# Performance work log

Measured on AMD Instinct MI355X. Metric: run time of the kernel, lower is better.

The kernel has to match this reference:

```python
import jax, jax.numpy as jnp
import numpy as np

B, T, S, D, H = 4, 1024, 1024, 1024, 16
DH = D // H  # head dim = 64
EPS = 1e-5
NEG = -1e9  # finite stand-in for -inf (grad-safe)


def setup_inputs() -> dict:
    key = jax.random.key(0)
    ks = jax.random.split(key, 9)
    std = D ** -0.5
    return {
        "q": jax.random.normal(ks[0], (B, T, D), jnp.float32),
        "k": jax.random.normal(ks[1], (B, S, D), jnp.float32),
        "v": jax.random.normal(ks[2], (B, S, D), jnp.float32),
        "attn_mask": jax.random.randint(ks[3], (T, S), 0, 2) == 1,
        "attn_bias": jax.random.normal(ks[4], (H, T, S), jnp.float32) * 0.1,
        "Wq": jax.random.normal(ks[5], (D, D), jnp.float32) * std,
        "Wk": jax.random.normal(ks[6], (D, D), jnp.float32) * std,
        "Wv": jax.random.normal(ks[7], (D, D), jnp.float32) * std,
        "Wo": jax.random.normal(ks[8], (D, D), jnp.float32) * std,
    }


def reference(q, k, v, attn_mask, attn_bias, Wq, Wk, Wv, Wo):
    # project and split heads: [B,T,D] -> [B,H,T,DH]
    qh = (q @ Wq.T).reshape(B, T, H, DH).transpose(0, 2, 1, 3) * (DH ** -0.5)
    kh = (k @ Wk.T).reshape(B, S, H, DH).transpose(0, 2, 1, 3)
    vh = (v @ Wv.T).reshape(B, S, H, DH).transpose(0, 2, 1, 3)
    # scores [B,H,T,S] with bias broadcast over batch, mask over (B,H)
    attn = jnp.einsum('bhtd,bhsd->bhts', qh, kh) + attn_bias
    attn = jnp.where(attn_mask, NEG, attn)
    # inverted softmax: normalize jointly over (heads, target) for each source pos
    a = jax.nn.softmax(attn.reshape(B, H * T, S), axis=1).reshape(B, H, T, S)
    a = jnp.where(attn_mask, 0.0, a)
    a = a / (a.sum(axis=-1, keepdims=True) + EPS)
    out = jnp.einsum('bhts,bhsd->bhtd', a, vh).transpose(0, 2, 1, 3).reshape(B, T, D)
    return out @ Wo.T
```

## Files before the change

### kernel.cpp

```cpp
#include <hip/hip_runtime.h>
#include <hip/hip_bf16.h>
#include <math.h>
#include <stdint.h>

#define B_ 4
#define T_ 1024
#define S_ 1024
#define D_ 1024
#define H_ 16
#define DH_ 64

static constexpr float EPSV = 1e-5f;
static constexpr float LOG2E = 1.4426950408889634f;
static constexpr float NEG2 = -1.4426950e9f;
static constexpr float SCALE_Q = 0.125f * LOG2E;

typedef __attribute__((ext_vector_type(8))) short short8;
typedef __attribute__((ext_vector_type(4))) float f32x4;

#define MFMA_BF16 __builtin_amdgcn_mfma_f32_16x16x32_bf16

__device__ __forceinline__ ushort f2bf(float f) {
  union { float f; unsigned u; } v; v.f = f;
  unsigned r = (v.u + 0x7FFFu + ((v.u >> 16) & 1u)) >> 16;
  return (ushort)r;
}
__device__ __forceinline__ float bf2f(ushort u) {
  union { unsigned u; float f; } v; v.u = (unsigned)u << 16;
  return v.f;
}
__device__ __forceinline__ float exp2_fast(float x) {
  float r;
  asm("v_exp_f32 %0, %1" : "=v"(r) : "v"(x));
  return r;
}
__device__ __forceinline__ unsigned cvt_pk_bf16(float lo, float hi) {
  unsigned r;
  asm("v_cvt_pk_bf16_f32 %0, %1, %2" : "=v"(r) : "v"(lo), "v"(hi));
  return r;
}

__device__ __forceinline__ void gl_lds16(const ushort* g, ushort* l) {
  __builtin_amdgcn_global_load_lds(
      (const __attribute__((address_space(1))) unsigned int*)g,
      (__attribute__((address_space(3))) unsigned int*)l, 16, 0, 0);
}

__global__ __launch_bounds__(256) void k_prep(
    const float* __restrict__ q, const float* __restrict__ k,
    const float* __restrict__ v, const float* __restrict__ Wq,
    const float* __restrict__ Wk, const float* __restrict__ Wv,
    const float* __restrict__ Wo, const float* __restrict__ bias,
    const int* __restrict__ mask, ushort* __restrict__ qb,
    ushort* __restrict__ kb, ushort* __restrict__ vb,
    ushort* __restrict__ Wqb, ushort* __restrict__ Wkb,
    ushort* __restrict__ Wvb, ushort* __restrict__ Wob,
    ushort* __restrict__ bm) {
  const int tid = threadIdx.x;
#pragma unroll 4
  for (int it = 0; it < 16; ++it) {
    const int tile = blockIdx.x + (it << 11);
    if (tile < 16384) {
      const float* src;
      ushort* dst;
      int local;
      if (tile < 12288) {
        const int which = tile >> 12;
        local = tile & 4095;
        src = (which == 0) ? q : (which == 1) ? k : v;
        dst = (which == 0) ? qb : (which == 1) ? kb : vb;
      } else {
        const int wv_ = tile - 12288;
        const int which = wv_ >> 10;
        local = wv_ & 1023;
        src = (which == 0) ? Wq : (which == 1) ? Wk : (which == 2) ? Wv : Wo;
        dst = (which == 0) ? Wqb : (which == 1) ? Wkb : (which == 2) ? Wvb : Wob;
      }
      const size_t base = (size_t)local * 1024 + tid * 4;
      float4 f = *(const float4*)(src + base);
      *(ushort4*)(dst + base) =
          make_ushort4(f2bf(f.x), f2bf(f.y), f2bf(f.z), f2bf(f.w));
    } else {
      const size_t base = (size_t)(tile - 16384) * 1024 + tid * 4;
      const size_t mi = base & (size_t)(T_ * S_ - 1);
      float4 b0 = *(const float4*)(bias + base);
      int4 m0 = *(const int4*)(mask + mi);
      ushort4 o = make_ushort4(f2bf(m0.x ? NEG2 : b0.x * LOG2E),
                               f2bf(m0.y ? NEG2 : b0.y * LOG2E),
                               f2bf(m0.z ? NEG2 : b0.z * LOG2E),
                               f2bf(m0.w ? NEG2 : b0.w * LOG2E));
      *(ushort4*)(bm + base) = o;
    }
  }
}

template <int MODE>
__global__ __launch_bounds__(256) void k_gemm(const ushort* __restrict__ A,
                                              const ushort* __restrict__ W,
                                              void* __restrict__ Yv,
                                              float scale) {
  __shared__ ushort At[128][32];
  __shared__ ushort Wt[128][32];
  const int tid = threadIdx.x;
  const int l = tid & 63, w = tid >> 6;
  const int wm = (w >> 1) * 64, wn = (w & 1) * 64;
  const int r16 = l & 15, g = l >> 4;
  const int i0 = blockIdx.x * 128, j0 = blockIdx.y * 128;
  const int srow = (l >> 2), scol = (l & 3) << 3;
  f32x4 acc[4][4] = {};

  for (int k0 = 0; k0 < D_; k0 += 32) {
    __syncthreads();
#pragma unroll
    for (int u = 0; u < 2; ++u) {
      const int row = w * 32 + u * 16 + srow;
      gl_lds16(&A[(size_t)(i0 + row) * D_ + k0 + scol], &At[w * 32 + u * 16][0]);
      gl_lds16(&W[(size_t)(j0 + row) * D_ + k0 + scol], &Wt[w * 32 + u * 16][0]);
    }
    __syncthreads();
    short8 a0[4], b0[4];
#pragma unroll
    for (int i = 0; i < 4; ++i) a0[i] = *(const short8*)&At[wm + 16 * i + r16][g * 8];
#pragma unroll
    for (int j = 0; j < 4; ++j) b0[j] = *(const short8*)&Wt[wn + 16 * j + r16][g * 8];
#pragma unroll
    for (int i = 0; i < 4; ++i)
#pragma unroll
      for (int j = 0; j < 4; ++j)
        acc[i][j] = MFMA_BF16(a0[i], b0[j], acc[i][j], 0, 0, 0);
  }

#pragma unroll
  for (int i = 0; i < 4; ++i)
#pragma unroll
    for (int j = 0; j < 4; ++j) {
      if (MODE == 2) {
        const int row0 = i0 + wm + 16 * i + 4 * g;
        const int col = j0 + wn + 16 * j + r16;
        const int bb = row0 >> 10, s = row0 & 1023;
        const int hh = col >> 6, dh = col & 63;
        ushort4 pw;
        pw.x = f2bf(acc[i][j][0] * scale); pw.y = f2bf(acc[i][j][1] * scale);
        pw.z = f2bf(acc[i][j][2] * scale); pw.w = f2bf(acc[i][j][3] * scale);
        *(ushort4*)&((ushort*)Yv)[((size_t)(bb * H_ + hh) * DH_ + dh) * 1024 + s] = pw;
      } else {
#pragma unroll
        for (int r = 0; r < 4; ++r) {
          const int row = i0 + wm + 16 * i + 4 * g + r;
          const int col = j0 + wn + 16 * j + r16;
          const float vv = acc[i][j][r] * scale;
          if (MODE == 0) {
            ((float*)Yv)[(size_t)row * D_ + col] = vv;
          } else {
            const int b = row >> 10, t = row & 1023;
            const int h = col >> 6, dh = col & 63;
            ((ushort*)Yv)[(((size_t)(b * H_ + h) * 1024) + t) * DH_ + dh] = f2bf(vv);
          }
        }
      }
    }
}

__global__ __launch_bounds__(256, 4) void k_colstats(const ushort* __restrict__ Qh,
                                                     const ushort* __restrict__ Kh,
                                                     const ushort* __restrict__ biasm,
                                                     float* __restrict__ pc) {
  __shared__ ushort Qt[128][72];
  __shared__ ushort U[9216];
  ushort (*Kt)[72] = (ushort(*)[72])U;
  typedef ushort Row144[144];
  Row144* Bm0 = (Row144*)U;
  Row144* Bm1 = (Row144*)(U + 4608);

  const int bid = blockIdx.x;
  const int x8 = bid & 7;
  const int b = (bid >> 3) & 3;
  const int v = (bid >> 5) * 8 + x8;
  const int h = v >> 6, st = (v >> 3) & 7, tt = v & 7;
  const int s0 = st * 128, t0 = tt * 128;
  const int tid = threadIdx.x, l = tid & 63, w = tid >> 6;
  const int r16 = l & 15, g = l >> 4;

  const ushort* qsrc = Qh + ((size_t)((b * H_ + h) * 1024) + t0) * DH_;
  const ushort* ksrc = Kh + ((size_t)((b * H_ + h) * 1024) + s0) * DH_;
#pragma unroll
  for (int u = 0; u < 4; ++u) {
    const int lin = u * 256 + tid;
    const int row = lin >> 3, c8 = (lin & 7) << 3;
    *(uint4*)&Qt[row][c8] = *(const uint4*)&qsrc[(size_t)row * DH_ + c8];
    *(uint4*)&Kt[row][c8] = *(const uint4*)&ksrc[(size_t)row * DH_ + c8];
  }
  __syncthreads();

  f32x4 acc[8][2] = {};
  __builtin_amdgcn_s_setprio(1);
#pragma unroll
  for (int kc = 0; kc < 2; ++kc) {
    short8 bk0 = *(const short8*)&Kt[w * 32 + r16][kc * 32 + g * 8];
    short8 bk1 = *(const short8*)&Kt[w * 32 + 16 + r16][kc * 32 + g * 8];
#pragma unroll
    for (int i = 0; i < 8; ++i) {
      short8 a = *(const short8*)&Qt[16 * i + r16][kc * 32 + g * 8];
      acc[i][0] = MFMA_BF16(a, bk0, acc[i][0], 0, 0, 0);
      acc[i][1] = MFMA_BF16(a, bk1, acc[i][1], 0, 0, 0);
    }
  }
  __builtin_amdgcn_s_setprio(0);
  __syncthreads();

  const ushort* bsrc = biasm + ((size_t)h * 1024 + t0) * 1024 + s0;
#pragma unroll
  for (int u = 0; u < 2; ++u) {
    const int lin = u * 256 + tid;
    const int row = lin >> 4, c8 = (lin & 15) << 3;
    *(uint4*)&Bm0[row][c8] = *(const uint4*)&bsrc[(size_t)row * 1024 + c8];
  }
  __syncthreads();

  float cs0 = 0.f, cs1 = 0.f;
  const int col0 = w * 32 + r16;
#pragma unroll
  for (int c = 0; c < 4; ++c) {
    Row144* cur = (c & 1) ? Bm1 : Bm0;
    if (c < 3) {
      Row144* nxt = (c & 1) ? Bm0 : Bm1;
#pragma unroll
      for (int u = 0; u < 2; ++u) {
        const int lin = u * 256 + tid;
        const int row = lin >> 4, c8 = (lin & 15) << 3;
        *(uint4*)&nxt[row][c8] =
            *(const uint4*)&bsrc[(size_t)((c + 1) * 32 + row) * 1024 + c8];
      }
    }
#pragma unroll
    for (int ii = 0; ii < 2; ++ii) {
      const int i = 2 * c + ii;
      const int lrow = 16 * ii + 4 * g;
#pragma unroll
      for (int r = 0; r < 4; ++r) {
        cs0 += exp2_fast(acc[i][0][r] + bf2f(cur[lrow + r][col0]));
        cs1 += exp2_fast(acc[i][1][r] + bf2f(cur[lrow + r][col0 + 16]));
      }
    }
    __syncthreads();
  }

  cs0 += __shfl_xor(cs0, 16); cs0 += __shfl_xor(cs0, 32);
  cs1 += __shfl_xor(cs1, 16); cs1 += __shfl_xor(cs1, 32);
  if (g == 0) {
    const size_t base = ((size_t)b * 1024 + s0 + col0) * 128 + h * 8 + tt;
    pc[base] = cs0;
    pc[base + 16 * 128] = cs1;
  }
}

__global__ __launch_bounds__(128) void k_combine(const float* __restrict__ pc,
                                                 float* __restrict__ Civ) {
  const int bs = blockIdx.x, tid = threadIdx.x;
  float c = pc[(size_t)bs * 128 + tid];
  __shared__ float sc[128];
  sc[tid] = c;
  __syncthreads();
  for (int off = 64; off > 0; off >>= 1) {
    if (tid < off) sc[tid] += sc[tid + off];
    __syncthreads();
  }
  if (tid == 0) {
    const float C = sc[0];
    Civ[bs] = (C > 0.f) ? 1.f / C : 0.f;
  }
}

__global__ __launch_bounds__(256, 2) void k_attn(const ushort* __restrict__ Qh,
                                                 const ushort* __restrict__ Kh,
                                                 const ushort* __restrict__ VhT,
                                                 const ushort* __restrict__ biasm,
                                                 const float* __restrict__ Civ,
                                                 ushort* __restrict__ O) {
  __shared__ ushort Kt[128][68];
  __shared__ ushort VtT[64][132];
  __shared__ ushort BmPt[128][132];
  __shared__ float Cih[128];
  __shared__ float Rp[4][128];

  const int bid = blockIdx.x;
  const int tt = bid >> 6;
  const int bh = bid & 63;
  const int b = bh >> 4, h = bh & 15;
  const int t0 = tt * 128;

  const int tid = threadIdx.x, l = tid & 63, w = tid >> 6;
  const int r16 = l & 15, g = l >> 4;
  const size_t kvbase = (size_t)bh * 1024 * DH_;
  const size_t vbase  = (size_t)bh * DH_ * 1024;

  short8 aq[8][2];
#pragma unroll
  for (int i = 0; i < 8; ++i) {
    const ushort* qr = Qh + ((size_t)bh * 1024 + t0 + 16 * i + r16) * DH_;
    aq[i][0] = *(const short8*)(qr + g * 8);
    aq[i][1] = *(const short8*)(qr + 32 + g * 8);
  }

  f32x4 aco[2][4] = {};
  float rloc[8] = {};

#pragma unroll 1
  for (int sc = 0; sc < 8; ++sc) {
    const int s0c = sc * 128;
    __syncthreads();

    {
      const ushort* ksrc = Kh + kvbase + (size_t)s0c * DH_;
#pragma unroll
      for (int u = 0; u < 4; ++u) {
        const int lin = u * 256 + tid;
        const int row = lin >> 3, c8 = (lin & 7) << 3;
        *(uint4*)&Kt[row][c8] = *(const uint4*)&ksrc[(size_t)row * DH_ + c8];
      }
      const ushort* vsrc = VhT + vbase + s0c;
#pragma unroll
      for (int u = 0; u < 4; ++u) {
        const int lin = u * 256 + tid;
        const int row = lin >> 4, c8 = (lin & 15) << 3;
        *(uint4*)&VtT[row][c8] = *(const uint4*)&vsrc[(size_t)row * 1024 + c8];
      }
      const ushort* bsrc = biasm + ((size_t)h * 1024 + t0) * 1024 + s0c;
#pragma unroll
      for (int u = 0; u < 8; ++u) {
        const int lin = u * 256 + tid;
        const int row = lin >> 4, c8 = (lin & 15) << 3;
        *(uint4*)&BmPt[row][c8] = *(const uint4*)&bsrc[(size_t)row * 1024 + c8];
      }
      if (tid < 128) Cih[tid] = Civ[(size_t)b * 1024 + s0c + tid];
    }
    __syncthreads();

#pragma unroll
    for (int j2 = 0; j2 < 2; ++j2) {
      const int jf = 2 * w + j2;
      f32x4 as[8] = {};
      short8 kf0 = *(const short8*)&Kt[16 * jf + r16][g * 8];
      short8 kf1 = *(const short8*)&Kt[16 * jf + r16][32 + g * 8];
      __builtin_amdgcn_s_setprio(1);
#pragma unroll
      for (int i = 0; i < 8; ++i) {
        as[i] = MFMA_BF16(kf0, aq[i][0], as[i], 0, 0, 0);
        as[i] = MFMA_BF16(kf1, aq[i][1], as[i], 0, 0, 0);
      }
      __builtin_amdgcn_s_setprio(0);
      const int scol = 16 * jf + 4 * g;
      const float4 cv = *(const float4*)&Cih[scol];
#pragma unroll
      for (int i = 0; i < 8; ++i) {
        const int srow = 16 * i + r16;
        ushort4 bv4 = *(const ushort4*)&BmPt[srow][scol];
        const float p0 = exp2_fast(as[i][0] + bf2f(bv4.x)) * cv.x;
        const float p1 = exp2_fast(as[i][1] + bf2f(bv4.y)) * cv.y;
        const float p2 = exp2_fast(as[i][2] + bf2f(bv4.z)) * cv.z;
        const float p3 = exp2_fast(as[i][3] + bf2f(bv4.w)) * cv.w;
        rloc[i] += (p0 + p1) + (p2 + p3);
        uint2 pw;
        pw.x = cvt_pk_bf16(p0, p1);
        pw.y = cvt_pk_bf16(p2, p3);
        *(uint2*)&BmPt[srow][scol] = pw;
      }
    }
    __syncthreads();

    __builtin_amdgcn_s_setprio(1);
#pragma unroll
    for (int rg = 0; rg < 2; ++rg) {
#pragma unroll
      for (int kc = 0; kc < 4; ++kc) {
        short8 ap = *(const short8*)&BmPt[32 * w + 16 * rg + r16][kc * 32 + g * 8];
#pragma unroll
        for (int j = 0; j < 4; ++j) {
          short8 bv = *(const short8*)&VtT[16 * j + r16][kc * 32 + g * 8];
          aco[rg][j] = MFMA_BF16(ap, bv, aco[rg][j], 0, 0, 0);
        }
      }
    }
    __builtin_amdgcn_s_setprio(0);
  }

#pragma unroll
  for (int i = 0; i < 8; ++i) {
    float vsum = rloc[i];
    vsum += __shfl_xor(vsum, 16);
    vsum += __shfl_xor(vsum, 32);
    if (l < 16) Rp[w][16 * i + r16] = vsum;
  }
  __syncthreads();

#pragma unroll
  for (int rg = 0; rg < 2; ++rg)
#pragma unroll
    for (int j = 0; j < 4; ++j)
#pragma unroll
      for (int r = 0; r < 4; ++r) {
        const int tl = 32 * w + 16 * rg + 4 * g + r;
        const float R = Rp[0][tl] + Rp[1][tl] + Rp[2][tl] + Rp[3][tl];
        const float o = aco[rg][j][r] / (R + EPSV);
        const int d = 16 * j + r16;
        O[((size_t)(b * 1024) + t0 + tl) * D_ + h * DH_ + d] = f2bf(o);
      }
}

extern "C" void kernel_launch(void* const* d_in, const int* in_sizes, int n_in,
                              void* d_out, int out_size, void* d_ws, size_t ws_size,
                              hipStream_t stream) {
  (void)in_sizes; (void)n_in; (void)out_size; (void)ws_size;
  const float* q    = (const float*)d_in[0];
  const float* k    = (const float*)d_in[1];
  const float* v    = (const float*)d_in[2];
  const int*   mask = (const int*)d_in[3];
  const float* bias = (const float*)d_in[4];
  const float* Wq   = (const float*)d_in[5];
  const float* Wk   = (const float*)d_in[6];
  const float* Wv   = (const float*)d_in[7];
  const float* Wo   = (const float*)d_in[8];
  float* out = (float*)d_out;

  ushort* qb   = (ushort*)d_ws;
  ushort* kb   = qb + 4194304;
  ushort* vb   = kb + 4194304;
  ushort* Wqb  = vb + 4194304;
  ushort* Wkb  = Wqb + 1048576;
  ushort* Wvb  = Wkb + 1048576;
  ushort* Wob  = Wvb + 1048576;
  ushort* Qh   = Wob + 1048576;
  ushort* Kh   = Qh + 4194304;
  ushort* VhT  = Kh + 4194304;
  ushort* Ob   = VhT + 4194304;
  ushort* bm   = Ob + 4194304;
  float*  pc   = (float*)(bm + 16777216);
  float*  Civ  = pc + 524288;

  k_prep<<<2048, 256, 0, stream>>>(q, k, v, Wq, Wk, Wv, Wo, bias, mask,
                                   qb, kb, vb, Wqb, Wkb, Wvb, Wob, bm);

  k_gemm<1><<<dim3(32, 8), 256, 0, stream>>>(qb, Wqb, Qh, SCALE_Q);
  k_gemm<1><<<dim3(32, 8), 256, 0, stream>>>(kb, Wkb, Kh, 1.0f);
  k_gemm<2><<<dim3(32, 8), 256, 0, stream>>>(vb, Wvb, VhT, 1.0f);

  k_colstats<<<4096, 256, 0, stream>>>(Qh, Kh, bm, pc);
  k_combine<<<4096, 128, 0, stream>>>(pc, Civ);
  k_attn<<<512, 256, 0, stream>>>(Qh, Kh, VhT, bm, Civ, Ob);

  k_gemm<0><<<dim3(32, 8), 256, 0, stream>>>(Ob, Wob, out, 1.0f);
}
```

Before: 195.1 us.

## Move bias/mask preprocessing into projection GEMM epilogues

The bias-plus-mask conversion to bf16 is taken out of the prep kernel and split across the three projection GEMM launches. Each of the 256 blocks converts 22 tiles after its GEMM work, so this memory-bound pass sits beside the compute-bound GEMMs. The prep kernel now only converts the inputs and weights, one tile per block across 16384 blocks. The risk is a longer GEMM tail, since each block runs the extra conversion serially after its matmul instead of in parallel with it.

New measurement: 221.9 us. 1.14x slower.

```diff
diff --git a/kernel.cpp b/kernel.cpp
--- a/kernel.cpp
+++ b/kernel.cpp
@@ -50,55 +50,40 @@
     const float* __restrict__ q, const float* __restrict__ k,
     const float* __restrict__ v, const float* __restrict__ Wq,
     const float* __restrict__ Wk, const float* __restrict__ Wv,
-    const float* __restrict__ Wo, const float* __restrict__ bias,
-    const int* __restrict__ mask, ushort* __restrict__ qb,
+    const float* __restrict__ Wo, ushort* __restrict__ qb,
     ushort* __restrict__ kb, ushort* __restrict__ vb,
     ushort* __restrict__ Wqb, ushort* __restrict__ Wkb,
-    ushort* __restrict__ Wvb, ushort* __restrict__ Wob,
-    ushort* __restrict__ bm) {
-  const int tid = threadIdx.x;
-#pragma unroll 4
-  for (int it = 0; it < 16; ++it) {
-    const int tile = blockIdx.x + (it << 11);
-    if (tile < 16384) {
-      const float* src;
-      ushort* dst;
-      int local;
-      if (tile < 12288) {
-        const int which = tile >> 12;
-        local = tile & 4095;
-        src = (which == 0) ? q : (which == 1) ? k : v;
-        dst = (which == 0) ? qb : (which == 1) ? kb : vb;
-      } else {
-        const int wv_ = tile - 12288;
-        const int which = wv_ >> 10;
-        local = wv_ & 1023;
-        src = (which == 0) ? Wq : (which == 1) ? Wk : (which == 2) ? Wv : Wo;
-        dst = (which == 0) ? Wqb : (which == 1) ? Wkb : (which == 2) ? Wvb : Wob;
-      }
-      const size_t base = (size_t)local * 1024 + tid * 4;
-      float4 f = *(const float4*)(src + base);
-      *(ushort4*)(dst + base) =
-          make_ushort4(f2bf(f.x), f2bf(f.y), f2bf(f.z), f2bf(f.w));
-    } else {
-      const size_t base = (size_t)(tile - 16384) * 1024 + tid * 4;
-      const size_t mi = base & (size_t)(T_ * S_ - 1);
-      float4 b0 = *(const float4*)(bias + base);
-      int4 m0 = *(const int4*)(mask + mi);
-      ushort4 o = make_ushort4(f2bf(m0.x ? NEG2 : b0.x * LOG2E),
-                               f2bf(m0.y ? NEG2 : b0.y * LOG2E),
-                               f2bf(m0.z ? NEG2 : b0.z * LOG2E),
-                               f2bf(m0.w ? NEG2 : b0.w * LOG2E));
-      *(ushort4*)(bm + base) = o;
-    }
-  }
-}
-
-template <int MODE>
+    ushort* __restrict__ Wvb, ushort* __restrict__ Wob) {
+  const int bid = blockIdx.x;
+  const float* src;
+  ushort* dst;
+  int local;
+  if (bid < 12288) {
+    const int which = bid >> 12;
+    local = bid & 4095;
+    src = (which == 0) ? q : (which == 1) ? k : v;
+    dst = (which == 0) ? qb : (which == 1) ? kb : vb;
+  } else {
+    const int wv_ = bid - 12288;
+    const int which = wv_ >> 10;
+    local = wv_ & 1023;
+    src = (which == 0) ? Wq : (which == 1) ? Wk : (which == 2) ? Wv : Wo;
+    dst = (which == 0) ? Wqb : (which == 1) ? Wkb : (which == 2) ? Wvb : Wob;
+  }
+  const int i = (local * 256 + threadIdx.x) * 4;
+  float4 t = *(const float4*)(src + i);
+  *(ushort4*)(dst + i) = make_ushort4(f2bf(t.x), f2bf(t.y), f2bf(t.z), f2bf(t.w));
+}
+
+template <int MODE, bool FUSE>
 __global__ __launch_bounds__(256) void k_gemm(const ushort* __restrict__ A,
                                               const ushort* __restrict__ W,
                                               void* __restrict__ Yv,
-                                              float scale) {
+                                              float scale,
+                                              const float* __restrict__ bias,
+                                              const int* __restrict__ mask,
+                                              ushort* __restrict__ bm,
+                                              int fuse_base) {
   __shared__ ushort At[128][32];
   __shared__ ushort Wt[128][32];
   const int tid = threadIdx.x;
@@ -159,6 +144,26 @@
         }
       }
     }
+
+  if (FUSE) {
+    const int blid = blockIdx.y * 32 + blockIdx.x;
+    const int tbase = fuse_base + blid * 22;
+#pragma unroll 2
+    for (int j = 0; j < 22; ++j) {
+      const int tile = tbase + j;
+      if (tile < 16384) {
+        const size_t base = (size_t)tile * 1024 + tid * 4;
+        const size_t mi = base & (size_t)(T_ * S_ - 1);
+        float4 b0 = *(const float4*)(bias + base);
+        int4 m0 = *(const int4*)(mask + mi);
+        ushort4 o = make_ushort4(f2bf(m0.x ? NEG2 : b0.x * LOG2E),
+                                 f2bf(m0.y ? NEG2 : b0.y * LOG2E),
+                                 f2bf(m0.z ? NEG2 : b0.z * LOG2E),
+                                 f2bf(m0.w ? NEG2 : b0.w * LOG2E));
+        *(ushort4*)(bm + base) = o;
+      }
+    }
+  }
 }
 
 __global__ __launch_bounds__(256, 4) void k_colstats(const ushort* __restrict__ Qh,
@@ -437,16 +442,20 @@
   float*  pc   = (float*)(bm + 16777216);
   float*  Civ  = pc + 524288;
 
-  k_prep<<<2048, 256, 0, stream>>>(q, k, v, Wq, Wk, Wv, Wo, bias, mask,
-                                   qb, kb, vb, Wqb, Wkb, Wvb, Wob, bm);
-
-  k_gemm<1><<<dim3(32, 8), 256, 0, stream>>>(qb, Wqb, Qh, SCALE_Q);
-  k_gemm<1><<<dim3(32, 8), 256, 0, stream>>>(kb, Wkb, Kh, 1.0f);
-  k_gemm<2><<<dim3(32, 8), 256, 0, stream>>>(vb, Wvb, VhT, 1.0f);
+  k_prep<<<16384, 256, 0, stream>>>(q, k, v, Wq, Wk, Wv, Wo,
+                                    qb, kb, vb, Wqb, Wkb, Wvb, Wob);
+
+  k_gemm<1, true><<<dim3(32, 8), 256, 0, stream>>>(qb, Wqb, Qh, SCALE_Q,
+                                                   bias, mask, bm, 0);
+  k_gemm<1, true><<<dim3(32, 8), 256, 0, stream>>>(kb, Wkb, Kh, 1.0f,
+                                                   bias, mask, bm, 5632);
+  k_gemm<2, true><<<dim3(32, 8), 256, 0, stream>>>(vb, Wvb, VhT, 1.0f,
+                                                   bias, mask, bm, 11264);
 
   k_colstats<<<4096, 256, 0, stream>>>(Qh, Kh, bm, pc);
   k_combine<<<4096, 128, 0, stream>>>(pc, Civ);
   k_attn<<<512, 256, 0, stream>>>(Qh, Kh, VhT, bm, Civ, Ob);
 
-  k_gemm<0><<<dim3(32, 8), 256, 0, stream>>>(Ob, Wob, out, 1.0f);
-}
+  k_gemm<0, false><<<dim3(32, 8), 256, 0, stream>>>(Ob, Wob, out, 1.0f,
+                                                    nullptr, nullptr, nullptr, -1);
+}
```
